# Performance work log

Measured on AMD Instinct MI355X. Metric: run time of the kernel, lower is better.

The kernel has to match this reference:

```python
import jax, jax.numpy as jnp
import numpy as np

BLOCK = 8
MIN_E, MAX_E = 0.2, 0.6
STRENGTH = 0.5


def dct_matrix(N):
    n = jnp.arange(N, dtype=jnp.float32)
    D = jnp.cos(jnp.pi * (2.0 * n[None, :] + 1.0) * n[:, None] / (2.0 * N))
    scale = jnp.where(n == 0, jnp.sqrt(1.0 / N), jnp.sqrt(2.0 / N))
    return D * scale[:, None]  # orthonormal DCT-II matrix [N,N]


def setup_inputs() -> dict:
    key = jax.random.key(0)
    k1, k2 = jax.random.split(key)
    cover = jax.random.uniform(k1, (8, 3, 512, 512), dtype=jnp.float32)
    secret_bits = jax.random.randint(k2, (8, 4096), 0, 2, dtype=jnp.int32)
    return {"cover": cover, "secret_bits": secret_bits}


def reference(cover, secret_bits):
    B, C, H, W = cover.shape
    bs = BLOCK
    nh, nw = H // bs, W // bs
    D = dct_matrix(bs)

    # blockify: [B,C,H,W] -> [B,C,nh,nw,bs,bs]
    blocks = cover.reshape(B, C, nh, bs, nw, bs).transpose(0, 1, 2, 4, 3, 5)
    # 2D orthonormal DCT per block: D @ X @ D^T
    dct_blocks = jnp.einsum('ij,bcnmjl,kl->bcnmik', D, blocks, D)

    # mid-frequency band selection mask over (u,v)
    u = jnp.arange(bs, dtype=jnp.float32)
    freq = (u[:, None] + u[None, :]) / (2.0 * (bs - 1))  # normalized in [0,1]
    freq_mask = (freq >= MIN_E) & (freq <= MAX_E)  # [bs,bs]

    # texture-adaptive block selection: per-block pixel variance
    var = jnp.var(blocks, axis=(-2, -1))  # [B,C,nh,nw]
    var_norm = (var - var.min()) / (var.max() - var.min() + 1e-8)
    thr = jnp.quantile(var_norm.reshape(-1), 0.3)
    tex_mask = var_norm > thr  # [B,C,nh,nw]

    sel = freq_mask[None, None, None, None, :, :] & tex_mask[..., None, None]
    sel_flat = sel.reshape(-1)

    # global row-major ordering of selected coefficients -> bit index
    order = jnp.cumsum(sel_flat.astype(jnp.int32)) - 1  # [N]
    num_bits = secret_bits.shape[1]
    eligible = sel_flat & (order < num_bits)

    per_b = C * nh * nw * bs * bs
    b_idx = jnp.arange(sel_flat.shape[0], dtype=jnp.int32) // per_b
    bit = secret_bits[b_idx, jnp.clip(order, 0, num_bits - 1)].astype(jnp.float32)

    coeff = dct_blocks.reshape(-1)
    rounded = jnp.round(coeff)
    lsb = jnp.mod(jnp.abs(rounded), 2.0)
    sign = jnp.where(coeff >= 0, 1.0, -1.0)
    delta = sign * (2.0 * bit - 1.0) * STRENGTH
    need_flip = eligible & (lsb != bit)
    modified = jnp.where(need_flip, coeff + delta, coeff)

    modified_blocks = modified.reshape(B, C, nh, nw, bs, bs)
    embedding_map = eligible.astype(jnp.float32).reshape(B, C, nh, nw, bs, bs)

    # inverse DCT: D^T @ Y @ D, then de-blockify
    pix = jnp.einsum('ji,bcnmjl,lk->bcnmik', D, modified_blocks, D)
    stego = pix.transpose(0, 1, 2, 4, 3, 5).reshape(B, C, H, W)
    return stego, embedding_map
```

## Files before the change

kernel.cpp:

```cpp
#include <hip/hip_runtime.h>

#define NBLK   98304
#define NPB    12288
#define HW     512
#define NUMBITS 4096
#define RANK0  29490
#define STEGO_N 6291456
#define ELIG   111
#define HISTB  512
#define CAPB   4096
#define NWGS   96

typedef unsigned long long ull;

struct DTab { double d[8][8]; };

constexpr double CT_[9] = {
  1.0,
  0.98078528040323044913,
  0.92387953251128675613,
  0.83146961230254523708,
  0.70710678118654752440,
  0.55557023301960222474,
  0.38268343236508977173,
  0.19509032201612826785,
  0.0
};
constexpr double cospi16(int m){
  int r = m % 32;
  return (r<=8) ? CT_[r] : (r<=16) ? -CT_[16-r] : (r<=24) ? -CT_[r-16] : CT_[32-r];
}
constexpr DTab make_dtab(){
  DTab t{};
  for(int k=0;k<8;k++) for(int n=0;n<8;n++){
    double s = (k==0) ? 0.35355339059327376220 : 0.5;
    t.d[k][n] = s * cospi16((2*n+1)*k);
  }
  return t;
}
constexpr DTab DT = make_dtab();

constexpr ull make_fmask(){
  ull m = 0;
  for(int u=0;u<8;u++) for(int v=0;v<8;v++){
    int s=u+v; if(s>=3 && s<=8) m |= (1ULL << (u*8+v));
  }
  return m;
}
constexpr ull FMASK = make_fmask();

__device__ __forceinline__ int binof(double v){
  int b = (int)(v * 2048.0);
  if(b > HISTB-1) b = HISTB-1;
  return b;
}

__device__ __forceinline__ void embed_one(const float* __restrict__ cover,
    const int* __restrict__ secret, float* __restrict__ out, int bi, int S2, int lane){
  int lr = lane>>3, lc = lane&7;
  int m = bi & 63, n = (bi>>6)&63, bc = bi>>12, bb = bi / NPB;
  const float* p  = cover + ((size_t)bc*HW + (size_t)n*8)*HW + (size_t)m*8;
  float*       po = out   + ((size_t)bc*HW + (size_t)n*8)*HW + (size_t)m*8;
  double x = (double)p[(size_t)lr*HW + lc];
  double t1 = 0.0;
#pragma unroll
  for(int j=0;j<8;j++) t1 += __shfl(x, lr*8+j) * DT.d[lc][j];
  double coef = 0.0;
#pragma unroll
  for(int k=0;k<8;k++) coef += DT.d[lr][k] * __shfl(t1, k*8+lc);
  bool sel = (FMASK>>lane)&1ULL;
  float mv = 0.f;
  if(sel){
    int fp  = (int)__popcll(FMASK & ((1ULL<<lane)-1ULL));
    int ord = 37*S2 + fp;
    if(ord < NUMBITS){
      mv = 1.f;
      double rnd = rint(coef);
      int lsb = ((int)fabs(rnd)) & 1;
      int bit = secret[(size_t)bb*NUMBITS + ord];
      if(lsb != bit) coef += ((coef>=0.0)?1.0:-1.0)*(2.0*(double)bit-1.0)*0.5;
    }
  }
  out[(size_t)STEGO_N + (size_t)bi*64 + lane] = mv;
  double t2 = 0.0;
#pragma unroll
  for(int u=0;u<8;u++) t2 += DT.d[u][lr] * __shfl(coef, u*8+lc);
  double px = 0.0;
#pragma unroll
  for(int qq=0;qq<8;qq++) px += __shfl(t2, lr*8+qq) * DT.d[qq][lc];
  po[(size_t)lr*HW + lc] = (float)px;
}

__global__ __launch_bounds__(512) void k_zero(unsigned* __restrict__ hist){
  hist[threadIdx.x] = 0u;
}

__global__ __launch_bounds__(256) void k_stats(const float* __restrict__ cover,
    float* __restrict__ out, double* __restrict__ var,
    unsigned* __restrict__ hist, ull* __restrict__ bucket){
  __shared__ unsigned h [HISTB];
  __shared__ unsigned h2[HISTB];
  __shared__ unsigned gb[HISTB];
  int tid = threadIdx.x;
  int i = blockIdx.x*256 + tid;
  for(int j=tid;j<HISTB;j+=256){ h[j]=0u; h2[j]=0u; }
  int m = i & 63, n = (i>>6)&63, bc = i>>12;
  const float* p  = cover + ((size_t)bc*HW + (size_t)n*8)*HW + (size_t)m*8;
  float*       po = out   + ((size_t)bc*HW + (size_t)n*8)*HW + (size_t)m*8;
  double s1=0.0, s2=0.0;
#pragma unroll
  for(int r=0;r<8;r++){
    const float4* q = (const float4*)(p + (size_t)r*HW);
    float4 a = q[0], b = q[1];
    float4* w = (float4*)(po + (size_t)r*HW);
    w[0]=a; w[1]=b;
    double x;
    x=(double)a.x; s1+=x; s2+=x*x;
    x=(double)a.y; s1+=x; s2+=x*x;
    x=(double)a.z; s1+=x; s2+=x*x;
    x=(double)a.w; s1+=x; s2+=x*x;
    x=(double)b.x; s1+=x; s2+=x*x;
    x=(double)b.y; s1+=x; s2+=x*x;
    x=(double)b.z; s1+=x; s2+=x*x;
    x=(double)b.w; s1+=x; s2+=x*x;
  }
  double mean = s1*(1.0/64.0);
  double v = s2*(1.0/64.0) - mean*mean;
  if(v < 0.0) v = 0.0;
  var[i] = v;
  float4 z = make_float4(0.f,0.f,0.f,0.f);
  float4* pm = (float4*)(out + (size_t)STEGO_N + (size_t)i*64);
#pragma unroll
  for(int j=0;j<16;j++) pm[j] = z;
  __syncthreads();
  int bn = binof(v);
  atomicAdd(&h[bn], 1u);
  __syncthreads();
  for(int j=tid;j<HISTB;j+=256){
    unsigned c = h[j];
    gb[j] = c ? atomicAdd(&hist[j], c) : 0u;
  }
  __syncthreads();
  unsigned slot = atomicAdd(&h2[bn], 1u);
  unsigned off  = gb[bn] + slot;
  if(off < CAPB) bucket[(size_t)bn*CAPB + off] = (ull)__double_as_longlong(v);
}

__global__ __launch_bounds__(1024) void k_embed(const float* __restrict__ cover,
    const int* __restrict__ secret, const double* __restrict__ var,
    const unsigned* __restrict__ hist, const ull* __restrict__ bucket,
    float* __restrict__ out){
  __shared__ ull scand[CAPB];
  __shared__ unsigned rhist[2048];
  __shared__ unsigned wsum[16];
  __shared__ int sdesc[3];
  __shared__ int spick[2];
  __shared__ int queue[ELIG];
  __shared__ unsigned wcnt[16];
  int tid = threadIdx.x, g = blockIdx.x;
  int lane = tid & 63, wid = tid >> 6;

  unsigned part = 0, incl = 0;
  if(tid < HISTB){
    part = hist[tid];
    incl = part;
#pragma unroll
    for(int off=1; off<64; off<<=1){
      unsigned t = __shfl_up(incl, off);
      if(lane >= off) incl += t;
    }
    if(lane==63) wsum[wid]=incl;
  }
  __syncthreads();
  if(tid < HISTB){
    unsigned wpre=0;
#pragma unroll
    for(int w=0;w<8;w++) if(w<wid) wpre += wsum[w];
    unsigned c = wpre + incl - part;
    if((unsigned)RANK0 >= c && (unsigned)RANK0 < c+part){
      sdesc[0]=tid; sdesc[1]=(int)c;
      sdesc[2]=(part < (unsigned)CAPB) ? (int)part : CAPB;
    }
  }
  __syncthreads();
  int b0 = sdesc[0], Cb = sdesc[1], K = sdesc[2];

  const ull* src = bucket + (size_t)b0*CAPB;
  for(int t=tid;t<K;t+=1024) scand[t]=src[t];
  __syncthreads();

  int rk = RANK0 - Cb;
  const int sh[6] = {55,44,33,22,11,0};
  ull pref = 0ULL;
  for(int r=0;r<6;r++){
    for(int j=tid;j<2048;j+=1024) rhist[j]=0u;
    __syncthreads();
    for(int t=tid;t<K;t+=1024){
      ull x = scand[t];
      bool match = (r==0) || ((x>>sh[r-1]) == (pref>>sh[r-1]));
      if(match) atomicAdd(&rhist[(unsigned)((x>>sh[r]) & 2047ULL)], 1u);
    }
    __syncthreads();
    unsigned a0 = rhist[2*tid], a1 = rhist[2*tid+1], p2 = a0+a1;
    unsigned inc2 = p2;
#pragma unroll
    for(int off=1; off<64; off<<=1){
      unsigned t = __shfl_up(inc2, off);
      if(lane >= off) inc2 += t;
    }
    if(lane==63) wsum[wid]=inc2;
    __syncthreads();
    unsigned wpre=0;
#pragma unroll
    for(int w=0;w<16;w++) if(w<wid) wpre += wsum[w];
    inc2 += wpre;
    unsigned excl = inc2 - p2;
    if((unsigned)rk >= excl && (unsigned)rk < inc2){
      if((unsigned)rk < excl + a0){ spick[0]=2*tid;   spick[1]=(int)excl; }
      else                        { spick[0]=2*tid+1; spick[1]=(int)(excl+a0); }
    }
    __syncthreads();
    pref |= ((ull)spick[0]) << sh[r];
    rk   -= spick[1];
    __syncthreads();
  }
  double A = __longlong_as_double((long long)pref);

  {
    int f = (var[tid] > A) ? 1 : 0;
    ull bal = __ballot(f);
    if(lane==0) wcnt[wid] = (unsigned)__popcll(bal);
    __syncthreads();
    int wpre=0, csum=0;
#pragma unroll
    for(int w=0;w<16;w++){
      int cc = (int)wcnt[w];
      if(w<wid) wpre += cc;
      csum += cc;
    }
    int P = wpre + (int)__popcll(bal & ((1ULL<<lane)-1ULL));
    if(f && P < ELIG) queue[P] = tid;
    __syncthreads();
    if(csum >= ELIG){
      int W = g*16 + wid;
      if(W < ELIG) embed_one(cover, secret, out, queue[W], W, lane);
      return;
    }
  }

  if(g != 0) return;
  __syncthreads();
  int total = 0;
  for(int chunk=0; chunk<96; chunk++){
    int ii = chunk*1024 + tid;
    int f = (var[ii] > A) ? 1 : 0;
    ull bal = __ballot(f);
    if(lane==0) wcnt[wid] = (unsigned)__popcll(bal);
    __syncthreads();
    int wpre=0, csum=0;
#pragma unroll
    for(int w=0;w<16;w++){
      int cc = (int)wcnt[w];
      if(w<wid) wpre += cc;
      csum += cc;
    }
    int P = total + wpre + (int)__popcll(bal & ((1ULL<<lane)-1ULL));
    if(f && P < ELIG) queue[P] = ii;
    total += csum;
    __syncthreads();
    if(total >= ELIG) break;
  }
  int nq = (total < ELIG) ? total : ELIG;
  for(int q = wid; q < nq; q += 16)
    embed_one(cover, secret, out, queue[q], q, lane);
}

extern "C" void kernel_launch(void* const* d_in, const int* in_sizes, int n_in,
                              void* d_out, int out_size, void* d_ws, size_t ws_size,
                              hipStream_t stream) {
  const float* cover  = (const float*)d_in[0];
  const int*   secret = (const int*)d_in[1];
  float* out = (float*)d_out;
  char*  ws  = (char*)d_ws;

  double*   var    = (double*)(ws);
  unsigned* hist   = (unsigned*)(ws + 786432);
  ull*      bucket = (ull*)(ws + 788480);

  k_zero <<<1,   512,  0, stream>>>(hist);
  k_stats<<<384, 256,  0, stream>>>(cover, out, var, hist, bucket);
  k_embed<<<NWGS,1024, 0, stream>>>(cover, secret, var, hist, bucket, out);
}
```

Baseline: 47.84 us.

## Replace global histogram atomics with per-workgroup partial histograms and buckets

k_stats now writes a 16-bit partial histogram and a small fixed-capacity bucket for each workgroup, with no global atomics. This removes the k_zero launch and the atomic contention on the global histogram. k_embed rebuilds the totals by summing the 384 partials per bin and gathers the candidates of the selected bin from the per-workgroup buckets. Workgroups whose bucket overflowed are rescanned from the variance array. The embed grid shrinks from 96 to 8 workgroups, which adds redundant reduction work in each workgroup.

```diff
diff --git a/kernel.cpp b/kernel.cpp
--- a/kernel.cpp
+++ b/kernel.cpp
@@ -9,7 +9,9 @@
 #define ELIG   111
 #define HISTB  512
 #define CAPB   4096
-#define NWGS   96
+#define CAP_WG 10
+#define NWG    384
+#define NEMB   8
 
 typedef unsigned long long ull;
 
@@ -91,18 +93,13 @@
   po[(size_t)lr*HW + lc] = (float)px;
 }
 
-__global__ __launch_bounds__(512) void k_zero(unsigned* __restrict__ hist){
-  hist[threadIdx.x] = 0u;
-}
-
 __global__ __launch_bounds__(256) void k_stats(const float* __restrict__ cover,
     float* __restrict__ out, double* __restrict__ var,
-    unsigned* __restrict__ hist, ull* __restrict__ bucket){
+    unsigned short* __restrict__ histp16, ull* __restrict__ bucket){
   __shared__ unsigned h [HISTB];
   __shared__ unsigned h2[HISTB];
-  __shared__ unsigned gb[HISTB];
-  int tid = threadIdx.x;
-  int i = blockIdx.x*256 + tid;
+  int tid = threadIdx.x, g = blockIdx.x;
+  int i = g*256 + tid;
   for(int j=tid;j<HISTB;j+=256){ h[j]=0u; h2[j]=0u; }
   int m = i & 63, n = (i>>6)&63, bc = i>>12;
   const float* p  = cover + ((size_t)bc*HW + (size_t)n*8)*HW + (size_t)m*8;
@@ -136,33 +133,40 @@
   int bn = binof(v);
   atomicAdd(&h[bn], 1u);
   __syncthreads();
-  for(int j=tid;j<HISTB;j+=256){
-    unsigned c = h[j];
-    gb[j] = c ? atomicAdd(&hist[j], c) : 0u;
-  }
-  __syncthreads();
+  for(int j=tid;j<HISTB;j+=256) histp16[(size_t)j*NWG + g] = (unsigned short)h[j];
   unsigned slot = atomicAdd(&h2[bn], 1u);
-  unsigned off  = gb[bn] + slot;
-  if(off < CAPB) bucket[(size_t)bn*CAPB + off] = (ull)__double_as_longlong(v);
+  if(slot < CAP_WG)
+    bucket[((size_t)bn*NWG + g)*CAP_WG + slot] = (ull)__double_as_longlong(v);
 }
 
 __global__ __launch_bounds__(1024) void k_embed(const float* __restrict__ cover,
     const int* __restrict__ secret, const double* __restrict__ var,
-    const unsigned* __restrict__ hist, const ull* __restrict__ bucket,
+    const unsigned short* __restrict__ histp16, const ull* __restrict__ bucket,
     float* __restrict__ out){
   __shared__ ull scand[CAPB];
   __shared__ unsigned rhist[2048];
   __shared__ unsigned wsum[16];
-  __shared__ int sdesc[3];
+  __shared__ int sdesc[2];
   __shared__ int spick[2];
+  __shared__ int scnt[NWG];
+  __shared__ int soff[NWG+1];
+  __shared__ int ovl[NWG];
+  __shared__ int s_nov;
   __shared__ int queue[ELIG];
   __shared__ unsigned wcnt[16];
   int tid = threadIdx.x, g = blockIdx.x;
   int lane = tid & 63, wid = tid >> 6;
+  if(tid==0) s_nov = 0;
 
   unsigned part = 0, incl = 0;
   if(tid < HISTB){
-    part = hist[tid];
+    const uint4* row = (const uint4*)(histp16 + (size_t)tid*NWG);
+#pragma unroll 8
+    for(int j=0;j<48;j++){
+      uint4 w4 = row[j];
+      part += (w4.x&0xFFFFu)+(w4.x>>16)+(w4.y&0xFFFFu)+(w4.y>>16)
+            + (w4.z&0xFFFFu)+(w4.z>>16)+(w4.w&0xFFFFu)+(w4.w>>16);
+    }
     incl = part;
 #pragma unroll
     for(int off=1; off<64; off<<=1){
@@ -177,16 +181,44 @@
 #pragma unroll
     for(int w=0;w<8;w++) if(w<wid) wpre += wsum[w];
     unsigned c = wpre + incl - part;
-    if((unsigned)RANK0 >= c && (unsigned)RANK0 < c+part){
-      sdesc[0]=tid; sdesc[1]=(int)c;
-      sdesc[2]=(part < (unsigned)CAPB) ? (int)part : CAPB;
-    }
-  }
-  __syncthreads();
-  int b0 = sdesc[0], Cb = sdesc[1], K = sdesc[2];
-
-  const ull* src = bucket + (size_t)b0*CAPB;
-  for(int t=tid;t<K;t+=1024) scand[t]=src[t];
+    if((unsigned)RANK0 >= c && (unsigned)RANK0 < c+part){ sdesc[0]=tid; sdesc[1]=(int)c; }
+  }
+  __syncthreads();
+  int b0 = sdesc[0], Cb = sdesc[1];
+
+  if(tid < NWG) scnt[tid] = (int)histp16[(size_t)b0*NWG + tid];
+  __syncthreads();
+  if(tid==0){
+    int c=0;
+    for(int w=0;w<NWG;w++){ soff[w]=c; c+=scnt[w]; }
+    soff[NWG]=c;
+  }
+  __syncthreads();
+  int K = soff[NWG]; if(K > CAPB) K = CAPB;
+  if(tid < NWG){
+    int c = scnt[tid], o = soff[tid];
+    if(c <= CAP_WG){
+      const ull* src = bucket + ((size_t)b0*NWG + tid)*CAP_WG;
+      for(int j=0;j<c;j++){ int d=o+j; if(d < CAPB) scand[d]=src[j]; }
+    }else{
+      int k = atomicAdd(&s_nov, 1);
+      ovl[k] = tid;
+    }
+  }
+  __syncthreads();
+  for(int ji=wid; ji<s_nov; ji+=16){
+    int w = ovl[ji];
+    int base = soff[w], cnt = 0;
+#pragma unroll
+    for(int r2=0;r2<4;r2++){
+      double v = var[w*256 + r2*64 + lane];
+      bool f = (binof(v)==b0);
+      ull bal = __ballot(f);
+      int pos = cnt + (int)__popcll(bal & ((1ULL<<lane)-1ULL));
+      if(f && base+pos < CAPB) scand[base+pos] = (ull)__double_as_longlong(v);
+      cnt += (int)__popcll(bal);
+    }
+  }
   __syncthreads();
 
   int rk = RANK0 - Cb;
@@ -283,11 +315,10 @@
   float* out = (float*)d_out;
   char*  ws  = (char*)d_ws;
 
-  double*   var    = (double*)(ws);
-  unsigned* hist   = (unsigned*)(ws + 786432);
-  ull*      bucket = (ull*)(ws + 788480);
-
-  k_zero <<<1,   512,  0, stream>>>(hist);
-  k_stats<<<384, 256,  0, stream>>>(cover, out, var, hist, bucket);
-  k_embed<<<NWGS,1024, 0, stream>>>(cover, secret, var, hist, bucket, out);
-}
+  double*         var     = (double*)(ws);
+  unsigned short* histp16 = (unsigned short*)(ws + 786432);
+  ull*            bucket  = (ull*)(ws + 1179648);
+
+  k_stats<<<NWG,  256,  0, stream>>>(cover, out, var, histp16, bucket);
+  k_embed<<<NEMB, 1024, 0, stream>>>(cover, secret, var, histp16, bucket, out);
+}
```

After: 59.71 us. 24.8% more time.
